# Kernel optimization log

Hardware: AMD Instinct MI355X
Metric: run time of the kernel (lower is better)

## Reference

```python
import jax, jax.numpy as jnp
import numpy as np

HW_SCALE = 64.0
B = 1048576  # batch of image pairs


def _forward_once(img, W_conv, W_linear):
    # img: (8, 8). Extract TL, TR, BL, BR 4x4 patches, each flattened to 16.
    # reshape->transpose gives quadrants in row-major order: TL, TR, BL, BR.
    patches = img.reshape(2, 4, 2, 4).transpose(0, 2, 1, 3).reshape(4, 16)
    acc1 = jax.nn.relu(patches @ W_conv)  # (4, 4)
    conv_out = jnp.clip(acc1 / HW_SCALE, -128.0, 127.0)
    # The original scalar double-loop writes conv_out row-major into row 0 of a
    # (4,16) zero matrix; rows 1-3 are zero, so the second matmul reduces to:
    acc2 = conv_out.reshape(16) @ W_linear  # (4,)
    return jnp.clip(acc2 / HW_SCALE, -128.0, 127.0)


def setup_inputs() -> dict:
    key = jax.random.key(0)
    k1, k2, k3, k4 = jax.random.split(key, 4)
    img1 = jax.random.normal(k1, (B, 8, 8), dtype=jnp.float32)
    img2 = jax.random.normal(k2, (B, 8, 8), dtype=jnp.float32)
    W_conv = jax.random.normal(k3, (16, 4), dtype=jnp.float32) * 0.1
    W_linear = jax.random.normal(k4, (16, 4), dtype=jnp.float32) * 0.1
    return {"img1": img1, "img2": img2, "W_conv": W_conv, "W_linear": W_linear}


def reference(img1, img2, W_conv, W_linear):
    f = jax.vmap(_forward_once, in_axes=(0, None, None))
    return f(img1, W_conv, W_linear), f(img2, W_conv, W_linear)
```

## Files before the change

### kernel.cpp

```cpp
#include <hip/hip_runtime.h>


typedef float fx4 __attribute__((ext_vector_type(4)));

static __device__ __forceinline__ fx4 ntload4(const fx4* __restrict__ p) {
    return __builtin_nontemporal_load(p);
}

static __device__ __forceinline__ fx4 forward_quad(
    fx4 v0, fx4 v1, fx4 v2, fx4 v3,
    const float4* __restrict__ wc4,
    float4 wl0, float4 wl1, float4 wl2, float4 wl3)
{
    const fx4 vv[4] = {v0, v1, v2, v3};
    float ax = 0.f, ay = 0.f, az = 0.f, aw = 0.f;
#pragma unroll
    for (int j = 0; j < 4; ++j) {
        const fx4 v = vv[j];
        const float4 w0 = wc4[4 * j + 0];
        const float4 w1 = wc4[4 * j + 1];
        const float4 w2 = wc4[4 * j + 2];
        const float4 w3 = wc4[4 * j + 3];
        ax = fmaf(v.x, w0.x, ax); ay = fmaf(v.x, w0.y, ay);
        az = fmaf(v.x, w0.z, az); aw = fmaf(v.x, w0.w, aw);
        ax = fmaf(v.y, w1.x, ax); ay = fmaf(v.y, w1.y, ay);
        az = fmaf(v.y, w1.z, az); aw = fmaf(v.y, w1.w, aw);
        ax = fmaf(v.z, w2.x, ax); ay = fmaf(v.z, w2.y, ay);
        az = fmaf(v.z, w2.z, az); aw = fmaf(v.z, w2.w, aw);
        ax = fmaf(v.w, w3.x, ax); ay = fmaf(v.w, w3.y, ay);
        az = fmaf(v.w, w3.z, az); aw = fmaf(v.w, w3.w, aw);
    }

    const float cox = fminf(fmaxf(fmaxf(ax, 0.f) * 0.015625f, -128.f), 127.f);
    const float coy = fminf(fmaxf(fmaxf(ay, 0.f) * 0.015625f, -128.f), 127.f);
    const float coz = fminf(fmaxf(fmaxf(az, 0.f) * 0.015625f, -128.f), 127.f);
    const float cow = fminf(fmaxf(fmaxf(aw, 0.f) * 0.015625f, -128.f), 127.f);

    float tx = fmaf(cox, wl0.x, fmaf(coy, wl1.x, fmaf(coz, wl2.x, cow * wl3.x)));
    float ty = fmaf(cox, wl0.y, fmaf(coy, wl1.y, fmaf(coz, wl2.y, cow * wl3.y)));
    float tz = fmaf(cox, wl0.z, fmaf(coy, wl1.z, fmaf(coz, wl2.z, cow * wl3.z)));
    float tw = fmaf(cox, wl0.w, fmaf(coy, wl1.w, fmaf(coz, wl2.w, cow * wl3.w)));

    tx += __shfl_xor(tx, 1); ty += __shfl_xor(ty, 1);
    tz += __shfl_xor(tz, 1); tw += __shfl_xor(tw, 1);
    tx += __shfl_xor(tx, 2); ty += __shfl_xor(ty, 2);
    tz += __shfl_xor(tz, 2); tw += __shfl_xor(tw, 2);

    fx4 o;
    o.x = fminf(fmaxf(tx * 0.015625f, -128.f), 127.f);
    o.y = fminf(fmaxf(ty * 0.015625f, -128.f), 127.f);
    o.z = fminf(fmaxf(tz * 0.015625f, -128.f), 127.f);
    o.w = fminf(fmaxf(tw * 0.015625f, -128.f), 127.f);
    return o;
}

__global__ __launch_bounds__(256, 4) void surrogate_kernel(
    const float* __restrict__ img1, const float* __restrict__ img2,
    const float* __restrict__ Wc,
    const float* __restrict__ Wl,
    float* __restrict__ out,
    int B)
{
    const int lane = threadIdx.x & 63;
    const int p    = lane & 3;
    const int mloc = lane >> 2;

    const float4* wc4 = (const float4*)Wc;
    const float4* wl4 = (const float4*)Wl;
    const float4 wl0 = wl4[p * 4 + 0];
    const float4 wl1 = wl4[p * 4 + 1];
    const float4 wl2 = wl4[p * 4 + 2];
    const float4 wl3 = wl4[p * 4 + 3];

    const int wavesPerBlock = blockDim.x >> 6;
    const int wid = (int)blockIdx.x * wavesPerBlock + ((int)threadIdx.x >> 6);
    const int nW  = (int)gridDim.x * wavesPerBlock;
    const long long total = 2LL * B;

    long long per = (total + nW - 1) / nW;
    per = ((per + 31) >> 5) << 5;
    const long long start = (long long)wid * per;
    long long end = start + per;
    if (end > total) end = total;

    const int cb = (p & 1) + ((p >> 1) << 3);
    fx4* __restrict__ out4 = (fx4*)out;

    long long g0 = start;
    for (; g0 + 32 <= end; g0 += 32) {
        const long long gA = g0 + mloc;
        const long long gB = g0 + 16 + mloc;
        const fx4* sA = (g0 < B)
            ? ((const fx4*)img1 + (gA << 4))
            : ((const fx4*)img2 + ((gA - B) << 4));
        const fx4* sB = (g0 + 16 < B)
            ? ((const fx4*)img1 + (gB << 4))
            : ((const fx4*)img2 + ((gB - B) << 4));

        const fx4 a0 = ntload4(sA + cb + 0);
        const fx4 a1 = ntload4(sA + cb + 2);
        const fx4 a2 = ntload4(sA + cb + 4);
        const fx4 a3 = ntload4(sA + cb + 6);
        const fx4 b0 = ntload4(sB + cb + 0);
        const fx4 b1 = ntload4(sB + cb + 2);
        const fx4 b2 = ntload4(sB + cb + 4);
        const fx4 b3 = ntload4(sB + cb + 6);

        const fx4 oA = forward_quad(a0, a1, a2, a3, wc4, wl0, wl1, wl2, wl3);
        const fx4 oB = forward_quad(b0, b1, b2, b3, wc4, wl0, wl1, wl2, wl3);

        if (p == 0) {
            __builtin_nontemporal_store(oA, out4 + gA);
            __builtin_nontemporal_store(oB, out4 + gB);
        }
    }
    if (g0 + 16 <= end) {
        const long long gA = g0 + mloc;
        const fx4* sA = (g0 < B)
            ? ((const fx4*)img1 + (gA << 4))
            : ((const fx4*)img2 + ((gA - B) << 4));
        const fx4 a0 = ntload4(sA + cb + 0);
        const fx4 a1 = ntload4(sA + cb + 2);
        const fx4 a2 = ntload4(sA + cb + 4);
        const fx4 a3 = ntload4(sA + cb + 6);
        const fx4 oA = forward_quad(a0, a1, a2, a3, wc4, wl0, wl1, wl2, wl3);
        if (p == 0) __builtin_nontemporal_store(oA, out4 + gA);
    }
}

extern "C" void kernel_launch(void* const* d_in, const int* in_sizes, int n_in,
                              void* d_out, int out_size, void* d_ws, size_t ws_size,
                              hipStream_t stream) {
    const float* img1 = (const float*)d_in[0];
    const float* img2 = (const float*)d_in[1];
    const float* Wc   = (const float*)d_in[2];
    const float* Wl   = (const float*)d_in[3];
    float* out = (float*)d_out;

    const int B = in_sizes[0] / 64;
    int blocks = (2 * B + 63) / 64;
    if (blocks > 2048) blocks = 2048;
    hipLaunchKernelGGL(surrogate_kernel, dim3(blocks), dim3(256), 0, stream,
                       img1, img2, Wc, Wl, out, B);
}
```

Baseline: 585.0 us.

## Switch to grid-stride 64-image chunks with deeper loads and plain memory ops

```diff
diff --git a/kernel.cpp b/kernel.cpp
--- a/kernel.cpp
+++ b/kernel.cpp
@@ -2,10 +2,6 @@
 
 
 typedef float fx4 __attribute__((ext_vector_type(4)));
-
-static __device__ __forceinline__ fx4 ntload4(const fx4* __restrict__ p) {
-    return __builtin_nontemporal_load(p);
-}
 
 static __device__ __forceinline__ fx4 forward_quad(
     fx4 v0, fx4 v1, fx4 v2, fx4 v3,
@@ -77,54 +73,52 @@
     const int nW  = (int)gridDim.x * wavesPerBlock;
     const long long total = 2LL * B;
 
-    long long per = (total + nW - 1) / nW;
-    per = ((per + 31) >> 5) << 5;
-    const long long start = (long long)wid * per;
-    long long end = start + per;
-    if (end > total) end = total;
-
     const int cb = (p & 1) + ((p >> 1) << 3);
     fx4* __restrict__ out4 = (fx4*)out;
 
-    long long g0 = start;
-    for (; g0 + 32 <= end; g0 += 32) {
-        const long long gA = g0 + mloc;
-        const long long gB = g0 + 16 + mloc;
-        const fx4* sA = (g0 < B)
-            ? ((const fx4*)img1 + (gA << 4))
-            : ((const fx4*)img2 + ((gA - B) << 4));
-        const fx4* sB = (g0 + 16 < B)
-            ? ((const fx4*)img1 + (gB << 4))
-            : ((const fx4*)img2 + ((gB - B) << 4));
+    const long long batchEnd = ((B & 63) == 0) ? (total & ~63LL) : 0;
+    const long long step = (long long)nW << 6;
 
-        const fx4 a0 = ntload4(sA + cb + 0);
-        const fx4 a1 = ntload4(sA + cb + 2);
-        const fx4 a2 = ntload4(sA + cb + 4);
-        const fx4 a3 = ntload4(sA + cb + 6);
-        const fx4 b0 = ntload4(sB + cb + 0);
-        const fx4 b1 = ntload4(sB + cb + 2);
-        const fx4 b2 = ntload4(sB + cb + 4);
-        const fx4 b3 = ntload4(sB + cb + 6);
+    for (long long g0 = (long long)wid << 6; g0 + 64 <= batchEnd; g0 += step) {
+        const long long gb = (g0 < B) ? g0 : g0 - B;
+        const fx4* __restrict__ src =
+            ((g0 < B) ? (const fx4*)img1 : (const fx4*)img2) + (gb << 4);
 
-        const fx4 oA = forward_quad(a0, a1, a2, a3, wc4, wl0, wl1, wl2, wl3);
-        const fx4 oB = forward_quad(b0, b1, b2, b3, wc4, wl0, wl1, wl2, wl3);
+        fx4 d[4][4];
+#pragma unroll
+        for (int s = 0; s < 4; ++s) {
+            const fx4* sp = src + (((s << 4) + mloc) << 4) + cb;
+            d[s][0] = sp[0];
+            d[s][1] = sp[2];
+            d[s][2] = sp[4];
+            d[s][3] = sp[6];
+        }
+
+        fx4 o[4];
+#pragma unroll
+        for (int s = 0; s < 4; ++s)
+            o[s] = forward_quad(d[s][0], d[s][1], d[s][2], d[s][3],
+                                wc4, wl0, wl1, wl2, wl3);
 
         if (p == 0) {
-            __builtin_nontemporal_store(oA, out4 + gA);
-            __builtin_nontemporal_store(oB, out4 + gB);
+#pragma unroll
+            for (int s = 0; s < 4; ++s)
+                out4[g0 + (s << 4) + mloc] = o[s];
         }
     }
-    if (g0 + 16 <= end) {
+
+    for (long long g0 = batchEnd + ((long long)wid << 4); g0 + 16 <= total;
+         g0 += (long long)nW << 4) {
         const long long gA = g0 + mloc;
         const fx4* sA = (g0 < B)
             ? ((const fx4*)img1 + (gA << 4))
             : ((const fx4*)img2 + ((gA - B) << 4));
-        const fx4 a0 = ntload4(sA + cb + 0);
-        const fx4 a1 = ntload4(sA + cb + 2);
-        const fx4 a2 = ntload4(sA + cb + 4);
-        const fx4 a3 = ntload4(sA + cb + 6);
-        const fx4 oA = forward_quad(a0, a1, a2, a3, wc4, wl0, wl1, wl2, wl3);
-        if (p == 0) __builtin_nontemporal_store(oA, out4 + gA);
+        const fx4 v0 = sA[cb + 0];
+        const fx4 v1 = sA[cb + 2];
+        const fx4 v2 = sA[cb + 4];
+        const fx4 v3 = sA[cb + 6];
+        const fx4 oA = forward_quad(v0, v1, v2, v3, wc4, wl0, wl1, wl2, wl3);
+        if (p == 0) out4[gA] = oA;
     }
 }
 
```

Result: faster. 520.2 us (-11.1%).
